# Kernel tuning notes

Hardware: AMD Instinct MI355X
Metric: run time of the kernel (lower is better)

The kernel has to match this reference:

```python
import jax, jax.numpy as jnp
import numpy as np

B, S, H, D = 4, 2048, 16, 1024  # batch, seq, heads, n_units
DK = D // H


def setup_inputs() -> dict:
    key = jax.random.key(0)
    ks = jax.random.split(key, 12)
    k_init = float(np.sqrt(1.0 / D))
    u = lambda k, shape: jax.random.uniform(k, shape, jnp.float32, -k_init, k_init)
    # causal mask, shared across batch/heads (True = attend)
    mask = jnp.broadcast_to(jnp.tril(jnp.ones((S, S), dtype=bool)), (B, S, S))
    return {
        "query": jax.random.normal(ks[0], (B, S, D), jnp.float32),
        "key": jax.random.normal(ks[1], (B, S, D), jnp.float32),
        "value": jax.random.normal(ks[2], (B, S, D), jnp.float32),
        "Wq": u(ks[3], (H, DK, D)), "bq": u(ks[4], (H, DK)),
        "Wk": u(ks[5], (H, DK, D)), "bk": u(ks[6], (H, DK)),
        "Wv": u(ks[7], (H, DK, D)), "bv": u(ks[8], (H, DK)),
        "Wp": u(ks[9], (D, D)), "bp": u(ks[10], (D,)),
        "mask": mask,
    }


def reference(query, key, value, Wq, bq, Wk, bk, Wv, bv, Wp, bp, mask):
    # per-head projections, batched over heads: [B,S,D] x [H,DK,D] -> [B,H,S,DK]
    Q = jnp.einsum('bsd,hkd->bhsk', query, Wq) + bq[None, :, None, :]
    K = jnp.einsum('bsd,hkd->bhsk', key, Wk) + bk[None, :, None, :]
    V = jnp.einsum('bsd,hkd->bhsk', value, Wv) + bv[None, :, None, :]
    scores = jnp.einsum('bhsk,bhtk->bhst', Q, K) / jnp.sqrt(jnp.float32(DK))
    scores = jnp.where(mask[:, None, :, :], scores, jnp.float32(-1e9))
    attn = jax.nn.softmax(scores, axis=-1)  # dropout disabled (eval)
    Z = jnp.einsum('bhst,bhtk->bhsk', attn, V)
    # concat heads on feature dim: [B,S,H*DK]
    Z = jnp.transpose(Z, (0, 2, 1, 3)).reshape(B, S, D)
    return Z @ Wp.T + bp
```

## Files before the change

### kernel.cpp

```cpp
#include <hip/hip_runtime.h>

typedef __bf16 bf16;
typedef __bf16 bf16x8 __attribute__((ext_vector_type(8)));
typedef float f32x4 __attribute__((ext_vector_type(4)));

#define BB 4
#define SS 2048
#define HH 16
#define DD 1024
#define DK 64
#define MTOT (BB * SS)

#define C1 0.18033688f
#define C2 -11.5415603f

#define MFMA16 __builtin_amdgcn_mfma_f32_16x16x32_bf16

__device__ __forceinline__ void gl_lds16(const bf16* g, bf16* l)
{
    __builtin_amdgcn_global_load_lds(
        (const __attribute__((address_space(1))) unsigned int*)g,
        (__attribute__((address_space(3))) unsigned int*)l, 16, 0, 0);
}

__global__ __launch_bounds__(256) void conv_kernel(
    const float* __restrict__ q, const float* __restrict__ k,
    const float* __restrict__ v,
    const float* __restrict__ wq, const float* __restrict__ wk,
    const float* __restrict__ wv, const float* __restrict__ wp,
    bf16* __restrict__ xdst, bf16* __restrict__ wdst)
{
    const float* src; bf16* d; size_t i;
    if (blockIdx.z < 3) {
        src = (blockIdx.z == 0) ? q : (blockIdx.z == 1) ? k : v;
        d = xdst + (size_t)blockIdx.z * ((size_t)MTOT * DD);
        i = ((size_t)blockIdx.x * 256 + threadIdx.x) * 8;
    } else {
        if (blockIdx.x >= 2048) return;
        const int wsel = blockIdx.x >> 9;
        src = (wsel == 0) ? wq : (wsel == 1) ? wk : (wsel == 2) ? wv : wp;
        d = wdst + (size_t)wsel * ((size_t)DD * DD);
        i = ((size_t)(blockIdx.x & 511) * 256 + threadIdx.x) * 8;
    }
    const float4 v0 = *(const float4*)(src + i);
    const float4 v1 = *(const float4*)(src + i + 4);
    bf16x8 r = { (bf16)v0.x, (bf16)v0.y, (bf16)v0.z, (bf16)v0.w,
                 (bf16)v1.x, (bf16)v1.y, (bf16)v1.z, (bf16)v1.w };
    *(bf16x8*)(d + i) = r;
}

__device__ __forceinline__ void qkv_read_bank(
    const bf16* __restrict__ sb, int kc, int ra, int rb,
    bf16x8 a[4], bf16x8 b[4])
{
    #pragma unroll
    for (int i = 0; i < 4; ++i)
        a[i] = *(const bf16x8*)&sb[kc * 8192 + ra + i * 512];
    #pragma unroll
    for (int j = 0; j < 4; ++j)
        b[j] = *(const bf16x8*)&sb[16384 + kc * 4096 + rb + j * 512];
}

__device__ __forceinline__ void qkv_mfma(
    f32x4 acc[4][4], const bf16x8 a[4], const bf16x8 b[4])
{
    __builtin_amdgcn_s_setprio(1);
    #pragma unroll
    for (int i = 0; i < 4; ++i)
        #pragma unroll
        for (int j = 0; j < 4; ++j)
            acc[i][j] = MFMA16(a[i], b[j], acc[i][j], 0, 0, 0);
    __builtin_amdgcn_s_setprio(0);
}

__device__ __forceinline__ void qkv_stage3(
    const bf16* __restrict__ srcA, const bf16* __restrict__ srcB,
    bf16* __restrict__ db, int X, int kc, int w)
{
    const bf16* sA = srcA + X * 64 + kc * 32;
    const bf16* sB = srcB + X * 64 + kc * 32;
    gl_lds16(sA,                    db + kc * 8192 + w * 512);
    gl_lds16(sA + (size_t)128 * DD, db + kc * 8192 + 4096 + w * 512);
    gl_lds16(sB,                    db + 16384 + kc * 4096 + w * 512);
}

__global__ __launch_bounds__(512, 2) void gemm_qkv(
    const bf16* __restrict__ x0, const bf16* __restrict__ x1,
    const bf16* __restrict__ x2, const bf16* __restrict__ w0,
    const bf16* __restrict__ w1, const bf16* __restrict__ w2,
    const float* __restrict__ bias0, const float* __restrict__ bias1,
    const float* __restrict__ bias2,
    bf16* __restrict__ o0, bf16* __restrict__ o1, bf16* __restrict__ o2)
{
    __shared__ __align__(16) bf16 smem[2 * 24576];

    const int z = blockIdx.z;
    const bf16* A = (z == 0) ? x0 : (z == 1) ? x1 : x2;
    const bf16* W = (z == 0) ? w0 : (z == 1) ? w1 : w2;
    const float* bias = (z == 0) ? bias0 : (z == 1) ? bias1 : bias2;
    bf16* out = (z == 0) ? o0 : (z == 1) ? o1 : o2;

    const int tid  = threadIdx.x;
    const int w    = tid >> 6;
    const int lane = tid & 63;
    const int quad = lane >> 4;
    const int lr   = lane & 15;
    const int wm   = w >> 1;
    const int wn   = w & 1;

    const int m_base = blockIdx.y * 256;
    const int n_base = blockIdx.x * 128;
    const int swz8 = (quad ^ ((lr >> 1) & 3)) * 8;

    const int ra = (wm * 64 + lr) * 32 + swz8;
    const int rb = (wn * 64 + lr) * 32 + swz8;

    const int c0 = ((tid & 3) ^ ((tid >> 3) & 3)) * 8;
    const bf16* srcA = A + (size_t)(m_base + (tid >> 2)) * DD + c0;
    const bf16* srcB = W + (size_t)(n_base + (tid >> 2)) * DD + c0;

    f32x4 acc[4][4];
    #pragma unroll
    for (int i = 0; i < 4; ++i)
        #pragma unroll
        for (int j = 0; j < 4; ++j)
            acc[i][j] = (f32x4){0.f, 0.f, 0.f, 0.f};

    bf16x8 a0[4], b0[4], a1[4], b1[4];

    qkv_stage3(srcA, srcB, smem,         0, 0, w);
    qkv_stage3(srcA, srcB, smem,         0, 1, w);
    qkv_stage3(srcA, srcB, smem + 24576, 1, 0, w);
    asm volatile("s_waitcnt vmcnt(6)" ::: "memory");
    __builtin_amdgcn_s_barrier();
    __builtin_amdgcn_sched_barrier(0);
    qkv_read_bank(smem, 0, ra, rb, a0, b0);

    for (int T = 0; T < 16; ++T) {
        bf16* cb = smem + (T & 1) * 24576;
        bf16* nb = smem + ((T + 1) & 1) * 24576;

        qkv_mfma(acc, a0, b0);
        if (T < 15) {
            qkv_stage3(srcA, srcB, nb, T + 1, 1, w);
            asm volatile("s_waitcnt vmcnt(6)" ::: "memory");
        } else {
            asm volatile("s_waitcnt vmcnt(0)" ::: "memory");
        }
        __builtin_amdgcn_sched_barrier(0);
        __builtin_amdgcn_s_barrier();
        __builtin_amdgcn_sched_barrier(0);
        qkv_read_bank(cb, 1, ra, rb, a1, b1);

        qkv_mfma(acc, a1, b1);
        if (T <= 13)
            qkv_stage3(srcA, srcB, cb, T + 2, 0, w);
        if (T < 15) {
            if (T <= 13) asm volatile("s_waitcnt vmcnt(6)" ::: "memory");
            else         asm volatile("s_waitcnt vmcnt(3)" ::: "memory");
            __builtin_amdgcn_sched_barrier(0);
            __builtin_amdgcn_s_barrier();
            __builtin_amdgcn_sched_barrier(0);
            qkv_read_bank(nb, 0, ra, rb, a0, b0);
        }
    }

    if (z == 2) {
        bf16* e = smem + w * 1216;
        const int h  = (blockIdx.x << 1) + wn;
        const int mg = m_base + wm * 64;
        const int b  = mg >> 11;
        const int s0 = mg & (SS - 1);
        #pragma unroll
        for (int j = 0; j < 4; ++j) {
            const float bb = bias[n_base + wn * 64 + j * 16 + lr];
            #pragma unroll
            for (int i = 0; i < 4; ++i)
                #pragma unroll
                for (int r = 0; r < 4; ++r)
                    e[lr * 76 + i * 16 + quad * 4 + r] = (bf16)(acc[i][j][r] + bb);
            #pragma unroll
            for (int p = 0; p < 2; ++p) {
                const int nn = p * 8 + (lane >> 3);
                const int mm = (lane & 7) * 8;
                const bf16x8 vv = *(const bf16x8*)&e[nn * 76 + mm];
                const int dk = j * 16 + nn;
                *(bf16x8*)(out + ((size_t)(b * HH + h) * DK + dk) * SS + s0 + mm) = vv;
            }
        }
    } else {
        #pragma unroll
        for (int j = 0; j < 4; ++j) {
            const int n  = n_base + wn * 64 + j * 16 + lr;
            const float bb = bias[n];
            const int hh = n >> 6;
            const int dk = n & (DK - 1);
            #pragma unroll
            for (int i = 0; i < 4; ++i)
                #pragma unroll
                for (int r = 0; r < 4; ++r) {
                    const int m = m_base + wm * 64 + i * 16 + quad * 4 + r;
                    const int bi = m >> 11, s = m & (SS - 1);
                    out[(((size_t)bi * HH + hh) * SS + s) * DK + dk]
                        = (bf16)(acc[i][j][r] + bb);
                }
        }
    }
}

template<int KC>
__device__ __forceinline__ void ophase(
    const bf16* __restrict__ sb, int wm, int wn, int lr, int swz8,
    f32x4 acc[4][4],
    const bf16* __restrict__ sA, const bf16* __restrict__ sB,
    bf16* __restrict__ db, int w, bool doStage)
{
    bf16x8 a[4], b[4];
    #pragma unroll
    for (int i = 0; i < 4; ++i)
        a[i] = *(const bf16x8*)&sb[KC * 8192 + (wm * 64 + i * 16 + lr) * 32 + swz8];
    #pragma unroll
    for (int j = 0; j < 4; ++j)
        b[j] = *(const bf16x8*)&sb[16384 + KC * 4096 + (wn * 64 + j * 16 + lr) * 32 + swz8];
    __builtin_amdgcn_sched_barrier(0);
    __builtin_amdgcn_s_barrier();
    asm volatile("s_waitcnt lgkmcnt(0)" ::: "memory");
    __builtin_amdgcn_sched_barrier(0);
    __builtin_amdgcn_s_setprio(1);
    #pragma unroll
    for (int i = 0; i < 4; ++i)
        #pragma unroll
        for (int j = 0; j < 4; ++j)
            acc[i][j] = __builtin_amdgcn_mfma_f32_16x16x32_bf16(
                            a[i], b[j], acc[i][j], 0, 0, 0);
    __builtin_amdgcn_s_setprio(0);
    if (doStage) {
        gl_lds16(sA + KC * 32,                    db + KC * 8192 + w * 512);
        gl_lds16(sA + KC * 32 + (size_t)128 * DD, db + KC * 8192 + 4096 + w * 512);
        gl_lds16(sB + KC * 32,                    db + 16384 + KC * 4096 + w * 512);
    }
    __builtin_amdgcn_sched_barrier(0);
}

__global__ __launch_bounds__(512, 2) void gemm_out(
    const bf16* __restrict__ A, const bf16* __restrict__ W,
    const float* __restrict__ bias, float* __restrict__ out)
{
    __shared__ __align__(16) bf16 smem[2 * 24576];

    const int tid  = threadIdx.x;
    const int w    = tid >> 6;
    const int lane = tid & 63;
    const int quad = lane >> 4;
    const int lr   = lane & 15;
    const int wm   = w >> 1;
    const int wn   = w & 1;

    const int m_base = blockIdx.y * 256;
    const int n_base = blockIdx.x * 128;
    const int swz8 = (quad ^ ((lr >> 1) & 3)) * 8;

    const int c0 = ((tid & 3) ^ ((tid >> 3) & 3)) * 8;
    const bf16* srcA = A + (size_t)(m_base + (tid >> 2)) * DD + c0;
    const bf16* srcB = W + (size_t)(n_base + (tid >> 2)) * DD + c0;

    f32x4 acc[4][4];
    #pragma unroll
    for (int i = 0; i < 4; ++i)
        #pragma unroll
        for (int j = 0; j < 4; ++j)
            acc[i][j] = (f32x4){0.f, 0.f, 0.f, 0.f};

    #pragma unroll
    for (int t = 0; t < 2; ++t) {
        bf16* db = smem + t * 24576;
        #pragma unroll
        for (int kc = 0; kc < 2; ++kc) {
            const bf16* sA = srcA + t * 64 + kc * 32;
            const bf16* sB = srcB + t * 64 + kc * 32;
            gl_lds16(sA,                      db + kc * 8192 + w * 512);
            gl_lds16(sA + (size_t)128 * DD,   db + kc * 8192 + 4096 + w * 512);
            gl_lds16(sB,                      db + 16384 + kc * 4096 + w * 512);
        }
    }
    asm volatile("s_waitcnt vmcnt(6)" ::: "memory");
    __builtin_amdgcn_s_barrier();

    #pragma unroll 2
    for (int T = 0; T < 16; ++T) {
        const bf16* sb = smem + (T & 1) * 24576;
        bf16* db = smem + (T & 1) * 24576;
        const bool st = (T + 2 < 16);
        const int tn = st ? (T + 2) : 0;
        const bf16* sA = srcA + tn * 64;
        const bf16* sB = srcB + tn * 64;

        ophase<0>(sb, wm, wn, lr, swz8, acc, sA, sB, db, w, st);
        __builtin_amdgcn_s_barrier();
        ophase<1>(sb, wm, wn, lr, swz8, acc, sA, sB, db, w, st);
        if (st) asm volatile("s_waitcnt vmcnt(6)" ::: "memory");
        else    asm volatile("s_waitcnt vmcnt(0)" ::: "memory");
        __builtin_amdgcn_s_barrier();
    }

    #pragma unroll
    for (int j = 0; j < 4; ++j) {
        const int n = n_base + wn * 64 + j * 16 + lr;
        const float bb = bias[n];
        #pragma unroll
        for (int i = 0; i < 4; ++i)
            #pragma unroll
            for (int r = 0; r < 4; ++r) {
                const int m = m_base + wm * 64 + i * 16 + quad * 4 + r;
                out[(size_t)m * DD + n] = acc[i][j][r] + bb;
            }
    }
}

template <bool DIAG>
__device__ __forceinline__ void attn_tile4(
    int quad, int lr, const bf16* __restrict__ Kc, const bf16* __restrict__ Vc,
    bf16* __restrict__ pb, const bf16x8 aq[2][2], const bf16x8& ones,
    f32x4 acc[2][4], f32x4 acc_l[2])
{
    bf16x8 kb[2][2];
    #pragma unroll
    for (int kvh = 0; kvh < 2; ++kvh)
        #pragma unroll
        for (int kc = 0; kc < 2; ++kc)
            kb[kvh][kc] = *(const bf16x8*)&Kc[
                ((kvh * 16 + lr) * 8 + ((kc * 4 + quad) ^ (lr & 7))) * 8];
    bf16x8 vb[4];
    #pragma unroll
    for (int c = 0; c < 4; ++c)
        vb[c] = *(const bf16x8*)&Vc[
            ((c * 16 + lr) * 4 + (quad ^ ((lr >> 1) & 3))) * 8];

    f32x4 s[2][2];
    #pragma unroll
    for (int h = 0; h < 2; ++h)
        #pragma unroll
        for (int kvh = 0; kvh < 2; ++kvh) {
            s[h][kvh] = (f32x4){0.f, 0.f, 0.f, 0.f};
            s[h][kvh] = __builtin_amdgcn_mfma_f32_16x16x32_bf16(
                            aq[h][0], kb[kvh][0], s[h][kvh], 0, 0, 0);
            s[h][kvh] = __builtin_amdgcn_mfma_f32_16x16x32_bf16(
                            aq[h][1], kb[kvh][1], s[h][kvh], 0, 0, 0);
        }

    #pragma unroll
    for (int h = 0; h < 2; ++h)
        #pragma unroll
        for (int kvh = 0; kvh < 2; ++kvh)
            #pragma unroll
            for (int r = 0; r < 4; ++r) {
                float p = exp2f(fmaf(s[h][kvh][r], C1, C2));
                if constexpr (DIAG) {
                    const bool ok = (kvh * 16 + lr) <= (h * 16 + quad * 4 + r);
                    p = ok ? p : 0.0f;
                }
                pb[(h * 16 + quad * 4 + r) * 40 + kvh * 16 + lr] = (bf16)p;
            }

    bf16x8 ap[2];
    #pragma unroll
    for (int h = 0; h < 2; ++h)
        ap[h] = *(const bf16x8*)&pb[(h * 16 + lr) * 40 + quad * 8];

    #pragma unroll
    for (int h = 0; h < 2; ++h)
        acc_l[h] = __builtin_amdgcn_mfma_f32_16x16x32_bf16(
                        ap[h], ones, acc_l[h], 0, 0, 0);
    #pragma unroll
    for (int c = 0; c < 4; ++c)
        #pragma unroll
        for (int h = 0; h < 2; ++h)
            acc[h][c] = __builtin_amdgcn_mfma_f32_16x16x32_bf16(
                            ap[h], vb[c], acc[h][c], 0, 0, 0);
}

__global__ __launch_bounds__(256, 4) void attn_kernel4(
    const bf16* __restrict__ q_ws, const bf16* __restrict__ k_ws,
    const bf16* __restrict__ v_ws, bf16* __restrict__ z_ws)
{
    __shared__ __align__(16) bf16 Kst[2][32 * 64];
    __shared__ __align__(16) bf16 Vst[2][64 * 32];
    __shared__ __align__(16) bf16 pbuf[4][32 * 40];

    const int tid  = threadIdx.x;
    const int w    = tid >> 6;
    const int lane = tid & 63;
    const int quad = lane >> 4;
    const int lr   = lane & 15;

    const int bh = blockIdx.x & 63;
    const int qg = 15 - (blockIdx.x >> 6);
    const int m0 = qg * 128 + w * 32;
    const int lim = 4 * qg + w;
    const int ntiles = 4 * qg + 4;

    const size_t base = (size_t)bh * SS * DK;
    const bf16* Kb = k_ws + base;
    const bf16* Vb = v_ws + base;
    bf16* pb = pbuf[w];

    const int krow = w * 8 + (lane >> 3);
    const int kcc  = (lane & 7) ^ ((lane >> 3) & 7);
    const bf16* ksrc = Kb + (size_t)krow * DK + kcc * 8;
    const int vrow = w * 16 + (lane >> 2);
    const int vcc  = (lane & 3) ^ ((lane >> 3) & 3);
    const bf16* vsrc = Vb + (size_t)vrow * SS + vcc * 8;

    bf16x8 aq[2][2];
    #pragma unroll
    for (int h = 0; h < 2; ++h)
        #pragma unroll
        for (int kc = 0; kc < 2; ++kc)
            aq[h][kc] = *(const bf16x8*)(q_ws + base
                + (size_t)(m0 + h * 16 + lr) * DK + kc * 32 + quad * 8);

    bf16x8 ones;
    #pragma unroll
    for (int i = 0; i < 8; ++i) ones[i] = (bf16)1.0f;

    f32x4 acc[2][4], acc_l[2];
    #pragma unroll
    for (int h = 0; h < 2; ++h) {
        acc_l[h] = (f32x4){0.f, 0.f, 0.f, 0.f};
        #pragma unroll
        for (int c = 0; c < 4; ++c) acc[h][c] = (f32x4){0.f, 0.f, 0.f, 0.f};
    }

    gl_lds16(ksrc, &Kst[0][w * 512]);
    gl_lds16(vsrc, &Vst[0][w * 512]);
    __syncthreads();

    for (int t = 0; t < ntiles; ++t) {
        if (t + 1 < ntiles) {
            gl_lds16(ksrc + (size_t)(t + 1) * 32 * DK, &Kst[(t + 1) & 1][w * 512]);
            gl_lds16(vsrc + (t + 1) * 32,              &Vst[(t + 1) & 1][w * 512]);
        }
        const bf16* Kc = Kst[t & 1];
        const bf16* Vc = Vst[t & 1];
        if (t < lim)
            attn_tile4<false>(quad, lr, Kc, Vc, pb, aq, ones, acc, acc_l);
        else if (t == lim)
            attn_tile4<true>(quad, lr, Kc, Vc, pb, aq, ones, acc, acc_l);
        __syncthreads();
    }

    const int b = bh >> 4, hh = bh & (HH - 1);
    #pragma unroll
    for (int h = 0; h < 2; ++h)
        #pragma unroll
        for (int r = 0; r < 4; ++r) {
            const float inv = 1.0f / acc_l[h][r];
            const int s = m0 + h * 16 + quad * 4 + r;
            #pragma unroll
            for (int c = 0; c < 4; ++c)
                z_ws[((size_t)(b * SS + s)) * DD + hh * DK + c * 16 + lr]
                    = (bf16)(acc[h][c][r] * inv);
        }
}

extern "C" void kernel_launch(void* const* d_in, const int* in_sizes, int n_in,
                              void* d_out, int out_size, void* d_ws, size_t ws_size,
                              hipStream_t stream)
{
    const float* query = (const float*)d_in[0];
    const float* key_  = (const float*)d_in[1];
    const float* value = (const float*)d_in[2];
    const float* Wq = (const float*)d_in[3];
    const float* bq = (const float*)d_in[4];
    const float* Wk = (const float*)d_in[5];
    const float* bk = (const float*)d_in[6];
    const float* Wv = (const float*)d_in[7];
    const float* bv = (const float*)d_in[8];
    const float* Wp = (const float*)d_in[9];
    const float* bp = (const float*)d_in[10];

    const size_t X = (size_t)MTOT * DD;
    const size_t W = (size_t)DD * DD;
    bf16* xq  = (bf16*)d_ws;
    bf16* xk  = xq + X;
    bf16* xv  = xk + X;
    bf16* wqb = xv + X;
    bf16* wkb = wqb + W;
    bf16* wvb = wkb + W;
    bf16* wpb = wvb + W;
    bf16* q_ws = wpb + W;
    bf16* k_ws = q_ws + X;
    bf16* v_ws = k_ws + X;
    bf16* z_ws = xq;

    conv_kernel<<<dim3(4096, 1, 4), 256, 0, stream>>>(
        query, key_, value, Wq, Wk, Wv, Wp, xq, wqb);

    gemm_qkv<<<dim3(8, 32, 3), 512, 0, stream>>>(
        xq, xk, xv, wqb, wkb, wvb, bq, bk, bv, q_ws, k_ws, v_ws);

    attn_kernel4<<<dim3(1024), 256, 0, stream>>>(q_ws, k_ws, v_ws, z_ws);

    gemm_out<<<dim3(8, 32), 512, 0, stream>>>(z_ws, wpb, bp, (float*)d_out);
}
```

Measured before the change: 358.0 us.

## Triple-buffer attention K/V tiles and share GEMM mainloop with output projection

New measurement: 348.9 us. 1.03x faster.

```diff
diff --git a/kernel.cpp b/kernel.cpp
--- a/kernel.cpp
+++ b/kernel.cpp
@@ -84,48 +84,10 @@
     gl_lds16(sB,                    db + 16384 + kc * 4096 + w * 512);
 }
 
-__global__ __launch_bounds__(512, 2) void gemm_qkv(
-    const bf16* __restrict__ x0, const bf16* __restrict__ x1,
-    const bf16* __restrict__ x2, const bf16* __restrict__ w0,
-    const bf16* __restrict__ w1, const bf16* __restrict__ w2,
-    const float* __restrict__ bias0, const float* __restrict__ bias1,
-    const float* __restrict__ bias2,
-    bf16* __restrict__ o0, bf16* __restrict__ o1, bf16* __restrict__ o2)
-{
-    __shared__ __align__(16) bf16 smem[2 * 24576];
-
-    const int z = blockIdx.z;
-    const bf16* A = (z == 0) ? x0 : (z == 1) ? x1 : x2;
-    const bf16* W = (z == 0) ? w0 : (z == 1) ? w1 : w2;
-    const float* bias = (z == 0) ? bias0 : (z == 1) ? bias1 : bias2;
-    bf16* out = (z == 0) ? o0 : (z == 1) ? o1 : o2;
-
-    const int tid  = threadIdx.x;
-    const int w    = tid >> 6;
-    const int lane = tid & 63;
-    const int quad = lane >> 4;
-    const int lr   = lane & 15;
-    const int wm   = w >> 1;
-    const int wn   = w & 1;
-
-    const int m_base = blockIdx.y * 256;
-    const int n_base = blockIdx.x * 128;
-    const int swz8 = (quad ^ ((lr >> 1) & 3)) * 8;
-
-    const int ra = (wm * 64 + lr) * 32 + swz8;
-    const int rb = (wn * 64 + lr) * 32 + swz8;
-
-    const int c0 = ((tid & 3) ^ ((tid >> 3) & 3)) * 8;
-    const bf16* srcA = A + (size_t)(m_base + (tid >> 2)) * DD + c0;
-    const bf16* srcB = W + (size_t)(n_base + (tid >> 2)) * DD + c0;
-
-    f32x4 acc[4][4];
-    #pragma unroll
-    for (int i = 0; i < 4; ++i)
-        #pragma unroll
-        for (int j = 0; j < 4; ++j)
-            acc[i][j] = (f32x4){0.f, 0.f, 0.f, 0.f};
-
+__device__ __forceinline__ void gemm_core(
+    const bf16* __restrict__ srcA, const bf16* __restrict__ srcB,
+    bf16* __restrict__ smem, int ra, int rb, int w, f32x4 acc[4][4])
+{
     bf16x8 a0[4], b0[4], a1[4], b1[4];
 
     qkv_stage3(srcA, srcB, smem,         0, 0, w);
@@ -164,6 +126,51 @@
             qkv_read_bank(nb, 0, ra, rb, a0, b0);
         }
     }
+}
+
+__global__ __launch_bounds__(512, 2) void gemm_qkv(
+    const bf16* __restrict__ x0, const bf16* __restrict__ x1,
+    const bf16* __restrict__ x2, const bf16* __restrict__ w0,
+    const bf16* __restrict__ w1, const bf16* __restrict__ w2,
+    const float* __restrict__ bias0, const float* __restrict__ bias1,
+    const float* __restrict__ bias2,
+    bf16* __restrict__ o0, bf16* __restrict__ o1, bf16* __restrict__ o2)
+{
+    __shared__ __align__(16) bf16 smem[2 * 24576];
+
+    const int z = blockIdx.z;
+    const bf16* A = (z == 0) ? x0 : (z == 1) ? x1 : x2;
+    const bf16* W = (z == 0) ? w0 : (z == 1) ? w1 : w2;
+    const float* bias = (z == 0) ? bias0 : (z == 1) ? bias1 : bias2;
+    bf16* out = (z == 0) ? o0 : (z == 1) ? o1 : o2;
+
+    const int tid  = threadIdx.x;
+    const int w    = tid >> 6;
+    const int lane = tid & 63;
+    const int quad = lane >> 4;
+    const int lr   = lane & 15;
+    const int wm   = w >> 1;
+    const int wn   = w & 1;
+
+    const int m_base = blockIdx.y * 256;
+    const int n_base = blockIdx.x * 128;
+    const int swz8 = (quad ^ ((lr >> 1) & 3)) * 8;
+
+    const int ra = (wm * 64 + lr) * 32 + swz8;
+    const int rb = (wn * 64 + lr) * 32 + swz8;
+
+    const int c0 = ((tid & 3) ^ ((tid >> 3) & 3)) * 8;
+    const bf16* srcA = A + (size_t)(m_base + (tid >> 2)) * DD + c0;
+    const bf16* srcB = W + (size_t)(n_base + (tid >> 2)) * DD + c0;
+
+    f32x4 acc[4][4];
+    #pragma unroll
+    for (int i = 0; i < 4; ++i)
+        #pragma unroll
+        for (int j = 0; j < 4; ++j)
+            acc[i][j] = (f32x4){0.f, 0.f, 0.f, 0.f};
+
+    gemm_core(srcA, srcB, smem, ra, rb, w, acc);
 
     if (z == 2) {
         bf16* e = smem + w * 1216;
@@ -208,40 +215,6 @@
     }
 }
 
-template<int KC>
-__device__ __forceinline__ void ophase(
-    const bf16* __restrict__ sb, int wm, int wn, int lr, int swz8,
-    f32x4 acc[4][4],
-    const bf16* __restrict__ sA, const bf16* __restrict__ sB,
-    bf16* __restrict__ db, int w, bool doStage)
-{
-    bf16x8 a[4], b[4];
-    #pragma unroll
-    for (int i = 0; i < 4; ++i)
-        a[i] = *(const bf16x8*)&sb[KC * 8192 + (wm * 64 + i * 16 + lr) * 32 + swz8];
-    #pragma unroll
-    for (int j = 0; j < 4; ++j)
-        b[j] = *(const bf16x8*)&sb[16384 + KC * 4096 + (wn * 64 + j * 16 + lr) * 32 + swz8];
-    __builtin_amdgcn_sched_barrier(0);
-    __builtin_amdgcn_s_barrier();
-    asm volatile("s_waitcnt lgkmcnt(0)" ::: "memory");
-    __builtin_amdgcn_sched_barrier(0);
-    __builtin_amdgcn_s_setprio(1);
-    #pragma unroll
-    for (int i = 0; i < 4; ++i)
-        #pragma unroll
-        for (int j = 0; j < 4; ++j)
-            acc[i][j] = __builtin_amdgcn_mfma_f32_16x16x32_bf16(
-                            a[i], b[j], acc[i][j], 0, 0, 0);
-    __builtin_amdgcn_s_setprio(0);
-    if (doStage) {
-        gl_lds16(sA + KC * 32,                    db + KC * 8192 + w * 512);
-        gl_lds16(sA + KC * 32 + (size_t)128 * DD, db + KC * 8192 + 4096 + w * 512);
-        gl_lds16(sB + KC * 32,                    db + 16384 + KC * 4096 + w * 512);
-    }
-    __builtin_amdgcn_sched_barrier(0);
-}
-
 __global__ __launch_bounds__(512, 2) void gemm_out(
     const bf16* __restrict__ A, const bf16* __restrict__ W,
     const float* __restrict__ bias, float* __restrict__ out)
@@ -260,6 +233,9 @@
     const int n_base = blockIdx.x * 128;
     const int swz8 = (quad ^ ((lr >> 1) & 3)) * 8;
 
+    const int ra = (wm * 64 + lr) * 32 + swz8;
+    const int rb = (wn * 64 + lr) * 32 + swz8;
+
     const int c0 = ((tid & 3) ^ ((tid >> 3) & 3)) * 8;
     const bf16* srcA = A + (size_t)(m_base + (tid >> 2)) * DD + c0;
     const bf16* srcB = W + (size_t)(n_base + (tid >> 2)) * DD + c0;
@@ -271,37 +247,7 @@
         for (int j = 0; j < 4; ++j)
             acc[i][j] = (f32x4){0.f, 0.f, 0.f, 0.f};
 
-    #pragma unroll
-    for (int t = 0; t < 2; ++t) {
-        bf16* db = smem + t * 24576;
-        #pragma unroll
-        for (int kc = 0; kc < 2; ++kc) {
-            const bf16* sA = srcA + t * 64 + kc * 32;
-            const bf16* sB = srcB + t * 64 + kc * 32;
-            gl_lds16(sA,                      db + kc * 8192 + w * 512);
-            gl_lds16(sA + (size_t)128 * DD,   db + kc * 8192 + 4096 + w * 512);
-            gl_lds16(sB,                      db + 16384 + kc * 4096 + w * 512);
-        }
-    }
-    asm volatile("s_waitcnt vmcnt(6)" ::: "memory");
-    __builtin_amdgcn_s_barrier();
-
-    #pragma unroll 2
-    for (int T = 0; T < 16; ++T) {
-        const bf16* sb = smem + (T & 1) * 24576;
-        bf16* db = smem + (T & 1) * 24576;
-        const bool st = (T + 2 < 16);
-        const int tn = st ? (T + 2) : 0;
-        const bf16* sA = srcA + tn * 64;
-        const bf16* sB = srcB + tn * 64;
-
-        ophase<0>(sb, wm, wn, lr, swz8, acc, sA, sB, db, w, st);
-        __builtin_amdgcn_s_barrier();
-        ophase<1>(sb, wm, wn, lr, swz8, acc, sA, sB, db, w, st);
-        if (st) asm volatile("s_waitcnt vmcnt(6)" ::: "memory");
-        else    asm volatile("s_waitcnt vmcnt(0)" ::: "memory");
-        __builtin_amdgcn_s_barrier();
-    }
+    gemm_core(srcA, srcB, smem, ra, rb, w, acc);
 
     #pragma unroll
     for (int j = 0; j < 4; ++j) {
@@ -342,10 +288,8 @@
         #pragma unroll
         for (int kvh = 0; kvh < 2; ++kvh) {
             s[h][kvh] = (f32x4){0.f, 0.f, 0.f, 0.f};
-            s[h][kvh] = __builtin_amdgcn_mfma_f32_16x16x32_bf16(
-                            aq[h][0], kb[kvh][0], s[h][kvh], 0, 0, 0);
-            s[h][kvh] = __builtin_amdgcn_mfma_f32_16x16x32_bf16(
-                            aq[h][1], kb[kvh][1], s[h][kvh], 0, 0, 0);
+            s[h][kvh] = MFMA16(aq[h][0], kb[kvh][0], s[h][kvh], 0, 0, 0);
+            s[h][kvh] = MFMA16(aq[h][1], kb[kvh][1], s[h][kvh], 0, 0, 0);
         }
 
     #pragma unroll
@@ -369,22 +313,20 @@
 
     #pragma unroll
     for (int h = 0; h < 2; ++h)
-        acc_l[h] = __builtin_amdgcn_mfma_f32_16x16x32_bf16(
-                        ap[h], ones, acc_l[h], 0, 0, 0);
+        acc_l[h] = MFMA16(ap[h], ones, acc_l[h], 0, 0, 0);
     #pragma unroll
     for (int c = 0; c < 4; ++c)
         #pragma unroll
         for (int h = 0; h < 2; ++h)
-            acc[h][c] = __builtin_amdgcn_mfma_f32_16x16x32_bf16(
-                            ap[h], vb[c], acc[h][c], 0, 0, 0);
+            acc[h][c] = MFMA16(ap[h], vb[c], acc[h][c], 0, 0, 0);
 }
 
 __global__ __launch_bounds__(256, 4) void attn_kernel4(
     const bf16* __restrict__ q_ws, const bf16* __restrict__ k_ws,
     const bf16* __restrict__ v_ws, bf16* __restrict__ z_ws)
 {
-    __shared__ __align__(16) bf16 Kst[2][32 * 64];
-    __shared__ __align__(16) bf16 Vst[2][64 * 32];
+    __shared__ __align__(16) bf16 Kst[3][32 * 64];
+    __shared__ __align__(16) bf16 Vst[3][64 * 32];
     __shared__ __align__(16) bf16 pbuf[4][32 * 40];
 
     const int tid  = threadIdx.x;
@@ -431,22 +373,30 @@
         for (int c = 0; c < 4; ++c) acc[h][c] = (f32x4){0.f, 0.f, 0.f, 0.f};
     }
 
-    gl_lds16(ksrc, &Kst[0][w * 512]);
-    gl_lds16(vsrc, &Vst[0][w * 512]);
-    __syncthreads();
-
+    gl_lds16(ksrc,                       &Kst[0][w * 512]);
+    gl_lds16(vsrc,                       &Vst[0][w * 512]);
+    gl_lds16(ksrc + (size_t)32 * DK,     &Kst[1][w * 512]);
+    gl_lds16(vsrc + 32,                  &Vst[1][w * 512]);
+
+    int cur = 0;
     for (int t = 0; t < ntiles; ++t) {
-        if (t + 1 < ntiles) {
-            gl_lds16(ksrc + (size_t)(t + 1) * 32 * DK, &Kst[(t + 1) & 1][w * 512]);
-            gl_lds16(vsrc + (t + 1) * 32,              &Vst[(t + 1) & 1][w * 512]);
-        }
-        const bf16* Kc = Kst[t & 1];
-        const bf16* Vc = Vst[t & 1];
+        if (t + 1 < ntiles) asm volatile("s_waitcnt vmcnt(2)" ::: "memory");
+        else                asm volatile("s_waitcnt vmcnt(0)" ::: "memory");
+        __builtin_amdgcn_s_barrier();
+        asm volatile("" ::: "memory");
+        __builtin_amdgcn_sched_barrier(0);
+        const bf16* Kc = Kst[cur];
+        const bf16* Vc = Vst[cur];
         if (t < lim)
             attn_tile4<false>(quad, lr, Kc, Vc, pb, aq, ones, acc, acc_l);
         else if (t == lim)
             attn_tile4<true>(quad, lr, Kc, Vc, pb, aq, ones, acc, acc_l);
-        __syncthreads();
+        if (t + 2 < ntiles) {
+            const int b2 = (cur + 2 >= 3) ? cur - 1 : cur + 2;
+            gl_lds16(ksrc + (size_t)(t + 2) * 32 * DK, &Kst[b2][w * 512]);
+            gl_lds16(vsrc + (t + 2) * 32,              &Vst[b2][w * 512]);
+        }
+        cur = (cur + 1 == 3) ? 0 : cur + 1;
     }
 
     const int b = bh >> 4, hh = bh & (HH - 1);
```
